# Performance work log

Measured on AMD Instinct MI355X. Metric: run time of the kernel, lower is better.

## Reference

```python
import jax, jax.numpy as jnp
import numpy as np

IN, OUT, HID = 1024, 1024, 2048
L = IN + OUT + HID
EPS = 1e-12  # F.normalize default eps


def _make_strength_matrix():
    fwd_s, bwd_s, lat_s, self_s = 1.0, 0.5, 0.3, 0.0
    i = np.arange(L)
    # torch: triu (incl diag) = forward, then tril (incl diag) = backward -> diag ends up backward here
    A = np.where(i[:, None] >= i[None, :], bwd_s, fwd_s).astype(np.float32)
    # lateral blocks (within input, within output, within hidden)
    A[0:IN, 0:IN] = lat_s
    A[IN:IN + OUT, IN:IN + OUT] = lat_s
    A[IN + OUT:L, IN + OUT:L] = lat_s
    A[i, i] = self_s
    return A


def setup_inputs() -> dict:
    key = jax.random.key(0)
    kx, ky, kw = jax.random.split(key, 3)
    B = 1024
    x = jax.random.normal(kx, (B, IN), dtype=jnp.float32)
    y = jax.random.normal(ky, (B, OUT), dtype=jnp.float32)
    W = jax.random.normal(kw, (L, L), dtype=jnp.float32) * 0.01
    idx = jnp.arange(L)
    W = W.at[idx, idx].set(0.0)  # fill_diagonal_(0) at init
    A = jnp.asarray(_make_strength_matrix())
    return {"x": x, "y": y, "W": W, "A": A, "n": 32}


def reference(x, y, W, A, n):
    # clamp_x=True, clamp_y=False, norm_hidden=True, average_window<=0
    B = x.shape[0]
    act0 = jnp.concatenate(
        [x, jnp.zeros_like(y), jnp.zeros((B, HID), dtype=x.dtype)], axis=1
    )  # [B, L]
    mw = W * A.T  # modified weights, loop-invariant

    def step(act, _):
        act = jax.nn.relu(act @ mw.T)          # linear(act, mw) + relu
        act = act.at[:, :IN].set(x)            # clamp_x
        hid = act[:, IN + OUT:]
        nrm = jnp.linalg.norm(hid, axis=1, keepdims=True)
        hid = hid / jnp.maximum(nrm, EPS)      # F.normalize p=2 dim=1
        act = act.at[:, IN + OUT:].set(hid)
        return act, None

    act, _ = jax.lax.scan(step, act0, None, length=n)
    return act
```

## Files before the change

kernel.cpp:

```cpp
#include <hip/hip_runtime.h>
#include <stdint.h>
#include <stddef.h>


#define L 4096
#define INX 1024
#define OUTX 1024
#define BATCH 1024
#define NCOL 3072
#define NITER 32

#define BM 64
#define BN 96
#define BK 64

typedef float floatx4 __attribute__((ext_vector_type(4)));
typedef short bf16x8 __attribute__((ext_vector_type(8)));

__device__ __forceinline__ unsigned short f2bf(float f) {
  unsigned int u = __float_as_uint(f);
  u += 0x7FFF + ((u >> 16) & 1);
  return (unsigned short)(u >> 16);
}
__device__ __forceinline__ float bf2f(unsigned short h) {
  return __uint_as_float(((unsigned int)h) << 16);
}

__device__ __forceinline__ void load_lds_16B(const void* g, void* s) {
  __builtin_amdgcn_global_load_lds(
      (const __attribute__((address_space(1))) unsigned int*)g,
      (__attribute__((address_space(3))) unsigned int*)s, 16, 0, 0);
}

__global__ void prep_mwn(const float* __restrict__ W, unsigned short* __restrict__ mwn) {
  int idx = blockIdx.x * 256 + threadIdx.x;
  int i = idx >> 10;
  int j4 = (idx & 1023) << 2;
  const float4 w = *(const float4*)&W[(size_t)(INX + i) * L + j4];
  const int c = INX + i;
  const int rc = (c < 2048) ? 1 : 2;
  float wv[4] = {w.x, w.y, w.z, w.w};
  unsigned short o[4];
#pragma unroll
  for (int k = 0; k < 4; ++k) {
    int j = j4 + k;
    int rj = (j < 1024) ? 0 : ((j < 2048) ? 1 : 2);
    float a = (j == c) ? 0.0f : ((rj == rc) ? 0.3f : ((j >= c) ? 0.5f : 1.0f));
    o[k] = f2bf(wv[k] * a);
  }
  *(ushort4*)&mwn[(size_t)i * L + j4] = make_ushort4(o[0], o[1], o[2], o[3]);
}

__global__ void init_act(const float* __restrict__ x, unsigned short* __restrict__ actA) {
  int i = blockIdx.x * 256 + threadIdx.x;
  int col = i & (L - 1), row = i >> 12;
  actA[i] = (col < INX) ? f2bf(x[(size_t)row * INX + col]) : (unsigned short)0;
}

__device__ __forceinline__ void stage(unsigned short* As, unsigned short* Bs,
                                      const unsigned short* gA, const unsigned short* gB,
                                      int kb, int t) {
  const int srow = t >> 3, schunk = t & 7;
  const int o = srow * BK + schunk * 8;
  load_lds_16B(gA + kb, &As[o]);
  load_lds_16B(gA + (size_t)32 * L + kb, &As[o + 32 * BK]);
  load_lds_16B(gB + kb, &Bs[o]);
  load_lds_16B(gB + (size_t)32 * L + kb, &Bs[o + 32 * BK]);
  load_lds_16B(gB + (size_t)64 * L + kb, &Bs[o + 64 * BK]);
}

__device__ __forceinline__ void mfma_step(const unsigned short* As, const unsigned short* Bs,
                                          int wm, int wn, int l15, int quad,
                                          floatx4 acc[2][3]) {
#pragma unroll
  for (int kk = 0; kk < 2; ++kk) {
    bf16x8 af[2], bfr[3];
    const int c = kk * 4 + quad;
#pragma unroll
    for (int mt = 0; mt < 2; ++mt) {
      int r = wm + mt * 16 + l15;
      af[mt] = *(const bf16x8*)&As[r * BK + ((c ^ (r & 7)) * 8)];
    }
#pragma unroll
    for (int nt = 0; nt < 3; ++nt) {
      int r = wn + nt * 16 + l15;
      bfr[nt] = *(const bf16x8*)&Bs[r * BK + ((c ^ (r & 7)) * 8)];
    }
#pragma unroll
    for (int mt = 0; mt < 2; ++mt)
#pragma unroll
      for (int nt = 0; nt < 3; ++nt)
        acc[mt][nt] = __builtin_amdgcn_mfma_f32_16x16x32_bf16(af[mt], bfr[nt],
                                                              acc[mt][nt], 0, 0, 0);
  }
}

#define PSTEP(s, R, D, ACC)                                                       \
  do {                                                                            \
    if ((s) < NS - 1) asm volatile("s_waitcnt vmcnt(5)" ::: "memory");            \
    else              asm volatile("s_waitcnt vmcnt(0)" ::: "memory");            \
    asm volatile("s_barrier" ::: "memory");                                       \
    if ((s) + 2 < NS) stage(As##D, Bs##D, gA, gB, KB0 + ((s) + 2) * BK, t);       \
    __builtin_amdgcn_s_setprio(1);                                                \
    mfma_step(As##R, Bs##R, wm, wn, l15, quad, ACC);                              \
    __builtin_amdgcn_s_setprio(0);                                                \
  } while (0)

template<int MODE>
__global__ __launch_bounds__(256, 2) void gemm_k(
    const unsigned short* __restrict__ act,
    const unsigned short* __restrict__ mwn,
    unsigned short* __restrict__ actn,
    unsigned short* __restrict__ c0,
    const float* __restrict__ nsq_prev,
    float* __restrict__ nsq_next) {
  __shared__ alignas(16) unsigned short As0[BM * BK], As1[BM * BK], As2[BM * BK];
  __shared__ alignas(16) unsigned short Bs0[BN * BK], Bs1[BN * BK], Bs2[BN * BK];
  const int t = threadIdx.x;
  const int lane = t & 63;
  const int wave = t >> 6;
  const int wm = (wave & 1) * 32;
  const int wn = (wave >> 1) * 48;
  const int l15 = lane & 15;
  const int quad = lane >> 4;

  const int b = blockIdx.y * 32 + blockIdx.x;
  const int n_idx = (b & 7) * 4 + (b >> 7);
  const int m_idx = (b >> 3) & 15;
  const int m0 = m_idx * BM;
  const int n0 = n_idx * BN;

  const int srow = t >> 3;
  const int schunk = t & 7;
  const int gchunk = schunk ^ (srow & 7);
  const unsigned short* gA = act + (size_t)(m0 + srow) * L + gchunk * 8;
  const unsigned short* gB = mwn + (size_t)(n0 + srow) * L + gchunk * 8;

  const int KB0 = MODE ? INX : 0;
  constexpr int NS = MODE ? 48 : 16;

  floatx4 accA[2][3], accB[2][3];
#pragma unroll
  for (int i = 0; i < 2; ++i)
#pragma unroll
    for (int j = 0; j < 3; ++j) {
      accA[i][j] = (floatx4){0.f, 0.f, 0.f, 0.f};
      if (MODE) accB[i][j] = (floatx4){0.f, 0.f, 0.f, 0.f};
    }

  stage(As0, Bs0, gA, gB, KB0, t);
  stage(As1, Bs1, gA, gB, KB0 + BK, t);

  PSTEP(0, 0, 2, accA);  PSTEP(1, 1, 0, accA);  PSTEP(2, 2, 1, accA);
  PSTEP(3, 0, 2, accA);  PSTEP(4, 1, 0, accA);  PSTEP(5, 2, 1, accA);
  PSTEP(6, 0, 2, accA);  PSTEP(7, 1, 0, accA);  PSTEP(8, 2, 1, accA);
  PSTEP(9, 0, 2, accA);  PSTEP(10, 1, 0, accA); PSTEP(11, 2, 1, accA);
  PSTEP(12, 0, 2, accA); PSTEP(13, 1, 0, accA); PSTEP(14, 2, 1, accA);
  PSTEP(15, 0, 2, accA);
  if (MODE) {
    PSTEP(16, 1, 0, accB); PSTEP(17, 2, 1, accB); PSTEP(18, 0, 2, accB);
    PSTEP(19, 1, 0, accB); PSTEP(20, 2, 1, accB); PSTEP(21, 0, 2, accB);
    PSTEP(22, 1, 0, accB); PSTEP(23, 2, 1, accB); PSTEP(24, 0, 2, accB);
    PSTEP(25, 1, 0, accB); PSTEP(26, 2, 1, accB); PSTEP(27, 0, 2, accB);
    PSTEP(28, 1, 0, accB); PSTEP(29, 2, 1, accB); PSTEP(30, 0, 2, accB);
    PSTEP(31, 1, 0, accB); PSTEP(32, 2, 1, accB); PSTEP(33, 0, 2, accB);
    PSTEP(34, 1, 0, accB); PSTEP(35, 2, 1, accB); PSTEP(36, 0, 2, accB);
    PSTEP(37, 1, 0, accB); PSTEP(38, 2, 1, accB); PSTEP(39, 0, 2, accB);
    PSTEP(40, 1, 0, accB); PSTEP(41, 2, 1, accB); PSTEP(42, 0, 2, accB);
    PSTEP(43, 1, 0, accB); PSTEP(44, 2, 1, accB); PSTEP(45, 0, 2, accB);
    PSTEP(46, 1, 0, accB); PSTEP(47, 2, 1, accB);
  }

  if (MODE == 0) {
    alignas(16) unsigned short buf[24];
#pragma unroll
    for (int mt = 0; mt < 2; ++mt)
#pragma unroll
      for (int nt = 0; nt < 3; ++nt)
#pragma unroll
        for (int r = 0; r < 4; ++r)
          buf[mt * 12 + nt * 4 + r] = f2bf(accA[mt][nt][r]);
    unsigned short* p = c0 + ((size_t)b * 256 + t) * 24;
    *(bf16x8*)&p[0]  = *(const bf16x8*)&buf[0];
    *(bf16x8*)&p[8]  = *(const bf16x8*)&buf[8];
    *(bf16x8*)&p[16] = *(const bf16x8*)&buf[16];
    return;
  }

  alignas(16) unsigned short c0s[24];
  {
    const unsigned short* p = c0 + ((size_t)b * 256 + t) * 24;
    *(bf16x8*)&c0s[0]  = *(const bf16x8*)&p[0];
    *(bf16x8*)&c0s[8]  = *(const bf16x8*)&p[8];
    *(bf16x8*)&c0s[16] = *(const bf16x8*)&p[16];
  }

  float sm[2][4];
#pragma unroll
  for (int mt = 0; mt < 2; ++mt)
#pragma unroll
    for (int r = 0; r < 4; ++r) {
      const int gm = m0 + wm + mt * 16 + quad * 4 + r;
      sm[mt][r] = 1.0f / fmaxf(sqrtf(nsq_prev[gm]), 1e-12f);
    }

  const bool has_hid = (n0 + BN) > OUTX;
#pragma unroll
  for (int mt = 0; mt < 2; ++mt) {
    float ss[4] = {0.f, 0.f, 0.f, 0.f};
#pragma unroll
    for (int nt = 0; nt < 3; ++nt) {
      const int gn = n0 + wn + nt * 16 + l15;
      const bool hid = gn >= OUTX;
#pragma unroll
      for (int r = 0; r < 4; ++r) {
        const int gm = m0 + wm + mt * 16 + quad * 4 + r;
        float v = bf2f(c0s[mt * 12 + nt * 4 + r]) + accA[mt][nt][r]
                  + sm[mt][r] * accB[mt][nt][r];
        v = fmaxf(v, 0.f);
        actn[(size_t)gm * L + INX + gn] = f2bf(v);
        if (hid) ss[r] += v * v;
      }
    }
    if (has_hid) {
#pragma unroll
      for (int r = 0; r < 4; ++r) {
        float sv = ss[r];
        sv += __shfl_xor(sv, 1);
        sv += __shfl_xor(sv, 2);
        sv += __shfl_xor(sv, 4);
        sv += __shfl_xor(sv, 8);
        if (l15 == 0)
          atomicAdd(&nsq_next[m0 + wm + mt * 16 + quad * 4 + r], sv);
      }
    }
  }
}

__global__ void finalize(const float* __restrict__ x, const unsigned short* __restrict__ act,
                         const float* __restrict__ nsq_fin, float* __restrict__ out) {
  int i = blockIdx.x * 256 + threadIdx.x;
  int col = i & (L - 1), row = i >> 12;
  float v;
  if (col < INX) {
    v = x[(size_t)row * INX + col];
  } else {
    v = bf2f(act[i]);
    if (col >= INX + OUTX) v *= 1.0f / fmaxf(sqrtf(nsq_fin[row]), 1e-12f);
  }
  out[i] = v;
}

extern "C" void kernel_launch(void* const* d_in, const int* in_sizes, int n_in,
                              void* d_out, int out_size, void* d_ws, size_t ws_size,
                              hipStream_t stream) {
  const float* x = (const float*)d_in[0];
  const float* W = (const float*)d_in[2];
  float* out = (float*)d_out;

  char* ws = (char*)d_ws;
  unsigned short* mwn  = (unsigned short*)(ws);
  unsigned short* actA = (unsigned short*)(ws + 25165824);
  unsigned short* actB = (unsigned short*)(ws + 33554432);
  unsigned short* c0   = (unsigned short*)(ws + 41943040);
  float* normsq        = (float*)(ws + 48234496);

  hipMemsetAsync(normsq, 0, (NITER + 1) * BATCH * sizeof(float), stream);
  prep_mwn<<<(NCOL * (L / 4)) / 256, 256, 0, stream>>>(W, mwn);
  init_act<<<(BATCH * L) / 256, 256, 0, stream>>>(x, actA);

  gemm_k<0><<<dim3(NCOL / BN, BATCH / BM), 256, 0, stream>>>(actA, mwn, nullptr, c0,
                                                             nullptr, nullptr);

  unsigned short* cur = actA;
  unsigned short* nxt = actB;
  for (int it = 0; it < NITER; ++it) {
    gemm_k<1><<<dim3(NCOL / BN, BATCH / BM), 256, 0, stream>>>(
        cur, mwn, nxt, c0, normsq + it * BATCH, normsq + (it + 1) * BATCH);
    unsigned short* tmp = cur; cur = nxt; nxt = tmp;
  }
  finalize<<<(BATCH * L) / 256, 256, 0, stream>>>(x, cur, normsq + NITER * BATCH, out);
}
```

Before: 1.110 ms.

## Split each K-step into two ping-pong phases with explicit barriers and scheduling fences

Each BK=64 K-step is split into two half-phases. Each half-phase first reads its LDS fragments, then issues part of the next stage's global-to-LDS loads (three loads, then two), waits on barriers and lgkmcnt, and runs the MFMAs inside sched_barrier fences at raised priority. The goal is to interleave LDS reads, global prefetch and MFMA issue more evenly so that waves alternate between memory and compute phases. It adds two extra barriers per K-step, and the partial vmcnt accounting is fragile. The grid dims are now hardcoded to 32x16, which equals the previous NCOL/BN by BATCH/BM.

```diff
diff --git a/kernel.cpp b/kernel.cpp
--- a/kernel.cpp
+++ b/kernel.cpp
@@ -57,53 +57,78 @@
   actA[i] = (col < INX) ? f2bf(x[(size_t)row * INX + col]) : (unsigned short)0;
 }
 
-__device__ __forceinline__ void stage(unsigned short* As, unsigned short* Bs,
-                                      const unsigned short* gA, const unsigned short* gB,
-                                      int kb, int t) {
+__device__ __forceinline__ void stage3(unsigned short* As, unsigned short* Bs,
+                                       const unsigned short* gA, const unsigned short* gB,
+                                       int kb, int t) {
   const int srow = t >> 3, schunk = t & 7;
   const int o = srow * BK + schunk * 8;
   load_lds_16B(gA + kb, &As[o]);
   load_lds_16B(gA + (size_t)32 * L + kb, &As[o + 32 * BK]);
   load_lds_16B(gB + kb, &Bs[o]);
+}
+__device__ __forceinline__ void stage2(unsigned short* Bs, const unsigned short* gB,
+                                       int kb, int t) {
+  const int srow = t >> 3, schunk = t & 7;
+  const int o = srow * BK + schunk * 8;
   load_lds_16B(gB + (size_t)32 * L + kb, &Bs[o + 32 * BK]);
   load_lds_16B(gB + (size_t)64 * L + kb, &Bs[o + 64 * BK]);
 }
 
-__device__ __forceinline__ void mfma_step(const unsigned short* As, const unsigned short* Bs,
-                                          int wm, int wn, int l15, int quad,
-                                          floatx4 acc[2][3]) {
-#pragma unroll
-  for (int kk = 0; kk < 2; ++kk) {
-    bf16x8 af[2], bfr[3];
-    const int c = kk * 4 + quad;
-#pragma unroll
-    for (int mt = 0; mt < 2; ++mt) {
-      int r = wm + mt * 16 + l15;
-      af[mt] = *(const bf16x8*)&As[r * BK + ((c ^ (r & 7)) * 8)];
-    }
-#pragma unroll
-    for (int nt = 0; nt < 3; ++nt) {
-      int r = wn + nt * 16 + l15;
-      bfr[nt] = *(const bf16x8*)&Bs[r * BK + ((c ^ (r & 7)) * 8)];
-    }
-#pragma unroll
-    for (int mt = 0; mt < 2; ++mt)
-#pragma unroll
-      for (int nt = 0; nt < 3; ++nt)
-        acc[mt][nt] = __builtin_amdgcn_mfma_f32_16x16x32_bf16(af[mt], bfr[nt],
-                                                              acc[mt][nt], 0, 0, 0);
-  }
-}
+struct FragK {
+  bf16x8 a[2];
+  bf16x8 b[3];
+};
+
+__device__ __forceinline__ void frag_read_kk(FragK& f, const unsigned short* As,
+                                             const unsigned short* Bs, int kk,
+                                             int wm, int wn, int l15, int quad) {
+  const int c = kk * 4 + quad;
+#pragma unroll
+  for (int mt = 0; mt < 2; ++mt) {
+    int r = wm + mt * 16 + l15;
+    f.a[mt] = *(const bf16x8*)&As[r * BK + ((c ^ (r & 7)) * 8)];
+  }
+#pragma unroll
+  for (int nt = 0; nt < 3; ++nt) {
+    int r = wn + nt * 16 + l15;
+    f.b[nt] = *(const bf16x8*)&Bs[r * BK + ((c ^ (r & 7)) * 8)];
+  }
+}
+
+__device__ __forceinline__ void phase_fma(const FragK& f, floatx4 acc[2][3]) {
+#pragma unroll
+  for (int mt = 0; mt < 2; ++mt)
+#pragma unroll
+    for (int nt = 0; nt < 3; ++nt)
+      acc[mt][nt] = __builtin_amdgcn_mfma_f32_16x16x32_bf16(f.a[mt], f.b[nt],
+                                                            acc[mt][nt], 0, 0, 0);
+}
+
+#define PPHASE(s, KK, R, D, ACC, ST3, ST2, WAITSTMT)                              \
+  do {                                                                            \
+    FragK fk_;                                                                    \
+    frag_read_kk(fk_, As##R, Bs##R, KK, wm, wn, l15, quad);                       \
+    if (ST3) stage3(As##D, Bs##D, gA, gB, KB0 + ((s) + 2) * BK, t);               \
+    if (ST2) stage2(Bs##D, gB, KB0 + ((s) + 2) * BK, t);                          \
+    WAITSTMT;                                                                     \
+    asm volatile("s_barrier" ::: "memory");                                       \
+    asm volatile("s_waitcnt lgkmcnt(0)" ::: "memory");                            \
+    __builtin_amdgcn_sched_barrier(0);                                            \
+    __builtin_amdgcn_s_setprio(1);                                                \
+    phase_fma(fk_, ACC);                                                          \
+    __builtin_amdgcn_s_setprio(0);                                                \
+    __builtin_amdgcn_sched_barrier(0);                                            \
+    asm volatile("s_barrier" ::: "memory");                                       \
+  } while (0)
 
 #define PSTEP(s, R, D, ACC)                                                       \
   do {                                                                            \
-    if ((s) < NS - 1) asm volatile("s_waitcnt vmcnt(5)" ::: "memory");            \
-    else              asm volatile("s_waitcnt vmcnt(0)" ::: "memory");            \
-    asm volatile("s_barrier" ::: "memory");                                       \
-    if ((s) + 2 < NS) stage(As##D, Bs##D, gA, gB, KB0 + ((s) + 2) * BK, t);       \
-    __builtin_amdgcn_s_setprio(1);                                                \
-    mfma_step(As##R, Bs##R, wm, wn, l15, quad, ACC);                              \
-    __builtin_amdgcn_s_setprio(0);                                                \
+    PPHASE(s, 0, R, D, ACC, (s) + 2 < NS, 0, );                                   \
+    PPHASE(s, 1, R, D, ACC, 0, (s) + 2 < NS,                                      \
+           if ((s) + 2 < NS) { asm volatile("s_waitcnt vmcnt(5)" ::: "memory"); } \
+           else if ((s) == NS - 2) {                                              \
+             asm volatile("s_waitcnt vmcnt(0)" ::: "memory");                     \
+           });                                                                    \
   } while (0)
 
 template<int MODE>
@@ -148,8 +173,12 @@
       if (MODE) accB[i][j] = (floatx4){0.f, 0.f, 0.f, 0.f};
     }
 
-  stage(As0, Bs0, gA, gB, KB0, t);
-  stage(As1, Bs1, gA, gB, KB0 + BK, t);
+  stage3(As0, Bs0, gA, gB, KB0, t);
+  stage2(Bs0, gB, KB0, t);
+  stage3(As1, Bs1, gA, gB, KB0 + BK, t);
+  stage2(Bs1, gB, KB0 + BK, t);
+  asm volatile("s_waitcnt vmcnt(5)" ::: "memory");
+  asm volatile("s_barrier" ::: "memory");
 
   PSTEP(0, 0, 2, accA);  PSTEP(1, 1, 0, accA);  PSTEP(2, 2, 1, accA);
   PSTEP(3, 0, 2, accA);  PSTEP(4, 1, 0, accA);  PSTEP(5, 2, 1, accA);
@@ -269,13 +298,13 @@
   prep_mwn<<<(NCOL * (L / 4)) / 256, 256, 0, stream>>>(W, mwn);
   init_act<<<(BATCH * L) / 256, 256, 0, stream>>>(x, actA);
 
-  gemm_k<0><<<dim3(NCOL / BN, BATCH / BM), 256, 0, stream>>>(actA, mwn, nullptr, c0,
-                                                             nullptr, nullptr);
+  gemm_k<0><<<dim3(32, 16), 256, 0, stream>>>(actA, mwn, nullptr, c0,
+                                              nullptr, nullptr);
 
   unsigned short* cur = actA;
   unsigned short* nxt = actB;
   for (int it = 0; it < NITER; ++it) {
-    gemm_k<1><<<dim3(NCOL / BN, BATCH / BM), 256, 0, stream>>>(
+    gemm_k<1><<<dim3(32, 16), 256, 0, stream>>>(
         cur, mwn, nxt, c0, normsq + it * BATCH, normsq + (it + 1) * BATCH);
     unsigned short* tmp = cur; cur = nxt; nxt = tmp;
   }
```

Measured after the change: 1.172 ms. 1.06x slower.
